# Optimization experiments

Hardware: AMD Instinct MI355X
Metric: run time of the kernel (lower is better)

Reference implementation:

```python
import jax, jax.numpy as jnp
import numpy as np

K = 9                 # kernel_size (num_points)
CENTER = K // 2
EXTEND_SCOPE = 1.0
EPS = 1e-5
GROUPS = 4            # out_ch // 4


def _cumsum_from_center(o):
    # o: [N, K, D, W, H]; serial offset accumulation outward from center row,
    # vectorized as two cumsums (matches the torch for-loop recurrence).
    upper = jnp.cumsum(o[:, CENTER:], axis=1)                                   # rows c..K-1
    lower = jnp.flip(jnp.cumsum(jnp.flip(o[:, :CENTER + 1], axis=1), axis=1), axis=1)  # rows 0..c
    return jnp.concatenate([lower[:, :CENTER], upper], axis=1)


def _coordinate_map_3d(offset):
    # offset: [N, 3K, D, W, H] -> (z, y, x) coord maps, each [N, D, W, H*K]  (morph=0, if_offset=True)
    N, _, D, W, H = offset.shape
    dt = offset.dtype
    z_off, y_off, _x_off = jnp.split(offset, 3, axis=1)   # each [N, K, D, W, H]
    z_acc = _cumsum_from_center(z_off)
    y_acc = _cumsum_from_center(y_off)
    z_c = jnp.arange(D, dtype=dt)[None, None, :, None, None]
    y_c = jnp.arange(W, dtype=dt)[None, None, None, :, None]
    x_c = jnp.arange(H, dtype=dt)[None, None, None, None, :]
    x_g = (jnp.arange(K, dtype=dt) - CENTER)[None, :, None, None, None]  # linspace(-c, c, K)
    z_new = z_c + EXTEND_SCOPE * z_acc                 # [N, K, D, W, H]
    y_new = y_c + EXTEND_SCOPE * y_acc
    x_new = jnp.broadcast_to(x_c + x_g, z_new.shape)

    def pack(a):  # [N,K,D,W,H] -> [N,D,W,H*K] (permute(0,4,1,5,2,6,3) + reshape in torch)
        return jnp.transpose(a, (0, 2, 3, 4, 1)).reshape(N, D, W, H * K)

    return pack(z_new), pack(y_new), pack(x_new)


def _trilinear_interpolate(feat, z, y, x):
    # feat: [N, C, D, W, H]; z/y/x: [N, D, W, HK] -> [N, C, D, W, HK]
    N, C, D, W, H = feat.shape
    featp = jnp.transpose(feat, (0, 2, 3, 4, 1))  # [N, D, W, H, C]
    z0 = jnp.clip(jnp.floor(z).astype(jnp.int32), 0, D - 1)
    z1 = jnp.clip(jnp.floor(z).astype(jnp.int32) + 1, 0, D - 1)
    y0 = jnp.clip(jnp.floor(y).astype(jnp.int32), 0, W - 1)
    y1 = jnp.clip(jnp.floor(y).astype(jnp.int32) + 1, 0, W - 1)
    x0 = jnp.clip(jnp.floor(x).astype(jnp.int32), 0, H - 1)
    x1 = jnp.clip(jnp.floor(x).astype(jnp.int32) + 1, 0, H - 1)
    z0f, z1f = z0.astype(feat.dtype), z1.astype(feat.dtype)
    y0f, y1f = y0.astype(feat.dtype), y1.astype(feat.dtype)
    x0f, x1f = x0.astype(feat.dtype), x1.astype(feat.dtype)
    b = jnp.arange(N)[:, None, None, None]

    def g(zi, yi, xi):
        return featp[b, zi, yi, xi]  # gather -> [N, D, W, HK, C]

    out = (g(z0, y0, x0) * ((z1f - z) * (y1f - y) * (x1f - x))[..., None]
         + g(z0, y0, x1) * ((z1f - z) * (y1f - y) * (x - x0f))[..., None]
         + g(z0, y1, x0) * ((z1f - z) * (y - y0f) * (x1f - x))[..., None]
         + g(z0, y1, x1) * ((z1f - z) * (y - y0f) * (x - x0f))[..., None]
         + g(z1, y0, x0) * ((z - z0f) * (y1f - y) * (x1f - x))[..., None]
         + g(z1, y0, x1) * ((z - z0f) * (y1f - y) * (x - x0f))[..., None]
         + g(z1, y1, x0) * ((z - z0f) * (y - y0f) * (x1f - x))[..., None]
         + g(z1, y1, x1) * ((z - z0f) * (y - y0f) * (x - x0f))[..., None])
    return jnp.transpose(out, (0, 4, 1, 2, 3))  # [N, C, D, W, HK]


def _conv3d(x, w, b, stride, padding):
    out = jax.lax.conv_general_dilated(x, w, window_strides=stride, padding=padding,
                                       dimension_numbers=('NCDHW', 'OIDHW', 'NCDHW'))
    return out + b[None, :, None, None, None]


def _batchnorm(x, gamma, beta):
    mu = jnp.mean(x, axis=(0, 2, 3, 4), keepdims=True)
    var = jnp.var(x, axis=(0, 2, 3, 4), keepdims=True)
    xn = (x - mu) * jax.lax.rsqrt(var + EPS)
    return gamma[None, :, None, None, None] * xn + beta[None, :, None, None, None]


def _groupnorm(x, gamma, beta):
    N, C = x.shape[:2]
    xg = x.reshape(N, GROUPS, C // GROUPS, *x.shape[2:])
    mu = jnp.mean(xg, axis=(2, 3, 4, 5), keepdims=True)
    var = jnp.var(xg, axis=(2, 3, 4, 5), keepdims=True)
    xn = ((xg - mu) * jax.lax.rsqrt(var + EPS)).reshape(x.shape)
    return gamma[None, :, None, None, None] * xn + beta[None, :, None, None, None]


def setup_inputs() -> dict:
    key = jax.random.key(0)
    ks = jax.random.split(key, 5)
    N, Cin, Cout, D, W, H = 1, 8, 16, 64, 64, 64
    f = jax.random.normal(ks[0], (N, Cin, D, W, H), dtype=jnp.float32)
    off_w = jax.random.normal(ks[1], (3 * K, Cin, 3, 3, 3), dtype=jnp.float32) * 0.05
    off_b = jax.random.normal(ks[2], (3 * K,), dtype=jnp.float32) * 0.05
    bn_g = jnp.ones((3 * K,), jnp.float32)
    bn_b = jnp.zeros((3 * K,), jnp.float32)
    dcn_w = jax.random.normal(ks[3], (Cout, Cin, 1, 1, K), dtype=jnp.float32) * 0.1
    dcn_b = jax.random.normal(ks[4], (Cout,), dtype=jnp.float32) * 0.05
    gn_g = jnp.ones((Cout,), jnp.float32)
    gn_b = jnp.zeros((Cout,), jnp.float32)
    return {"f": f, "off_w": off_w, "off_b": off_b, "bn_g": bn_g, "bn_b": bn_b,
            "dcn_w": dcn_w, "dcn_b": dcn_b, "gn_g": gn_g, "gn_b": gn_b}


def reference(f, off_w, off_b, bn_g, bn_b, dcn_w, dcn_b, gn_g, gn_b):
    # offset branch: Conv3d(in, 3K, 3, pad 1) -> BN -> tanh
    offset = _conv3d(f, off_w, off_b, (1, 1, 1), [(1, 1), (1, 1), (1, 1)])
    offset = jnp.tanh(_batchnorm(offset, bn_g, bn_b))
    # deformable coordinate map (morph=0) + trilinear gather
    z, y, x = _coordinate_map_3d(offset)
    deformed = _trilinear_interpolate(f, z, y, x)        # [N, C, D, W, H*K]
    # fused conv along the extended axis: kernel (1,1,K), stride (1,1,K)
    out = _conv3d(deformed, dcn_w, dcn_b, (1, 1, K), [(0, 0), (0, 0), (0, 0)])
    return jax.nn.relu(_groupnorm(out, gn_g, gn_b))      # [N, out, D, W, H]
```

## Files before the change

kernel.cpp:

```cpp
#include <hip/hip_runtime.h>
#include <math.h>

#define VOX 262144

__device__ __forceinline__ int clampi(int v, int lo, int hi) {
    return v < lo ? lo : (v > hi ? hi : v);
}

__global__ void k_init(float* __restrict__ stats) {
    if (threadIdx.x < 64) stats[threadIdx.x] = 0.f;
}

__global__ void k_wt(const float* __restrict__ w, float* __restrict__ wT) {
    int i = blockIdx.x * 256 + threadIdx.x;
    if (i < 3888) {
        int c = i / 216, r = i % 216;
        int ci = r / 27, k = r % 27;
        wT[(k * 8 + ci) * 18 + c] = w[i];
    }
}

__global__ void k_transpose(const float* __restrict__ f, float* __restrict__ ft) {
    int idx = blockIdx.x * 256 + threadIdx.x;
    int x = idx & 63, y = (idx >> 6) & 63, z = (idx >> 12) & 63, ci = idx >> 18;
    ft[(((z * 64 + y) * 64 + x) << 3) + ci] = f[idx];
}

__global__ __launch_bounds__(256) void k_conv_off(
        const float* __restrict__ f, const float* __restrict__ wT,
        const float* __restrict__ b, float* __restrict__ offs,
        float* __restrict__ stats) {
    int idx = blockIdx.x * 256 + threadIdx.x;
    int h = idx & 63, wy = (idx >> 6) & 63, d = idx >> 12;

    int hc0 = h > 0 ? h - 1 : 0;
    int hc2 = h < 63 ? h + 1 : 63;
    float mh0 = h > 0 ? 1.f : 0.f;
    float mh2 = h < 63 ? 1.f : 0.f;

    float acc[18];
#pragma unroll
    for (int c = 0; c < 18; c++) acc[c] = b[c];

#pragma unroll
    for (int kd = 0; kd < 3; kd++) {
        int dd = d + kd - 1;
#pragma unroll
        for (int kw = 0; kw < 3; kw++) {
            int ww = wy + kw - 1;
            bool ok = ((unsigned)dd < 64u) & ((unsigned)ww < 64u);
            const float* fp = f + (dd * 64 + ww) * 64;
            const float* wrow = wT + ((kd * 3 + kw) * 3) * 8 * 18;
            if (ok) {
#pragma unroll
                for (int ci = 0; ci < 8; ci++) {
                    float v0 = fp[ci * VOX + hc0] * mh0;
                    float v1 = fp[ci * VOX + h];
                    float v2 = fp[ci * VOX + hc2] * mh2;
                    const float* wp = wrow + ci * 18;
#pragma unroll
                    for (int c = 0; c < 18; c++) {
                        float a = acc[c];
                        a = fmaf(v0, wp[c], a);
                        a = fmaf(v1, wp[144 + c], a);
                        a = fmaf(v2, wp[288 + c], a);
                        acc[c] = a;
                    }
                }
            }
        }
    }

#pragma unroll
    for (int c = 0; c < 18; c++) offs[c * VOX + idx] = acc[c];

    __shared__ float ls[36];
    if (threadIdx.x < 36) ls[threadIdx.x] = 0.f;
    __syncthreads();
#pragma unroll
    for (int c = 0; c < 18; c++) {
        float s = acc[c], q = acc[c] * acc[c];
#pragma unroll
        for (int o = 32; o > 0; o >>= 1) {
            s += __shfl_xor(s, o);
            q += __shfl_xor(q, o);
        }
        if ((threadIdx.x & 63) == 0) {
            atomicAdd(&ls[c], s);
            atomicAdd(&ls[18 + c], q);
        }
    }
    __syncthreads();
    if (threadIdx.x < 36) atomicAdd(&stats[threadIdx.x], ls[threadIdx.x]);
}

__global__ __launch_bounds__(256) void k_main(
        const float* __restrict__ ft, const float* __restrict__ offs,
        const float* __restrict__ stats, const float* __restrict__ bn_g,
        const float* __restrict__ bn_b, const float* __restrict__ dw,
        const float* __restrict__ db, float* __restrict__ out,
        float* __restrict__ gstats) {
    int idx = blockIdx.x * 256 + threadIdx.x;
    int h = idx & 63, wy = (idx >> 6) & 63, d = idx >> 12;
    const float inv = 1.f / (float)VOX;

    float zo[9], yo[9];
#pragma unroll
    for (int c = 0; c < 18; c++) {
        float m = stats[c] * inv;
        float var = stats[18 + c] * inv - m * m;
        float rs = rsqrtf(var + 1e-5f);
        float t = tanhf(bn_g[c] * ((offs[c * VOX + idx] - m) * rs) + bn_b[c]);
        if (c < 9) zo[c] = t; else yo[c - 9] = t;
    }

    float za[9], ya[9];
    za[4] = zo[4]; ya[4] = yo[4];
#pragma unroll
    for (int k = 5; k < 9; k++) { za[k] = za[k - 1] + zo[k]; ya[k] = ya[k - 1] + yo[k]; }
#pragma unroll
    for (int k = 3; k >= 0; k--) { za[k] = za[k + 1] + zo[k]; ya[k] = ya[k + 1] + yo[k]; }

    float acc[16];
#pragma unroll
    for (int co = 0; co < 16; co++) acc[co] = db[co];

#pragma unroll
    for (int k = 0; k < 9; k++) {
        int xi = h + k - 4;
        if (xi >= 0 && xi <= 62) {
            float z = (float)d + za[k];
            float y = (float)wy + ya[k];
            float fz = floorf(z), fy = floorf(y);
            int iz = (int)fz, iy = (int)fy;
            int z0 = clampi(iz, 0, 63), z1 = clampi(iz + 1, 0, 63);
            int y0 = clampi(iy, 0, 63), y1 = clampi(iy + 1, 0, 63);
            float wz0 = (float)z1 - z, wz1 = z - (float)z0;
            float wy0 = (float)y1 - y, wy1 = y - (float)y0;
            float w00 = wz0 * wy0, w01 = wz0 * wy1, w10 = wz1 * wy0, w11 = wz1 * wy1;

            const float4* p00 = (const float4*)(ft + (((z0 * 64 + y0) * 64 + xi) << 3));
            const float4* p01 = (const float4*)(ft + (((z0 * 64 + y1) * 64 + xi) << 3));
            const float4* p10 = (const float4*)(ft + (((z1 * 64 + y0) * 64 + xi) << 3));
            const float4* p11 = (const float4*)(ft + (((z1 * 64 + y1) * 64 + xi) << 3));
            float4 a00 = p00[0], b00 = p00[1];
            float4 a01 = p01[0], b01 = p01[1];
            float4 a10 = p10[0], b10 = p10[1];
            float4 a11 = p11[0], b11 = p11[1];

            float v[8];
            v[0] = w00 * a00.x + w01 * a01.x + w10 * a10.x + w11 * a11.x;
            v[1] = w00 * a00.y + w01 * a01.y + w10 * a10.y + w11 * a11.y;
            v[2] = w00 * a00.z + w01 * a01.z + w10 * a10.z + w11 * a11.z;
            v[3] = w00 * a00.w + w01 * a01.w + w10 * a10.w + w11 * a11.w;
            v[4] = w00 * b00.x + w01 * b01.x + w10 * b10.x + w11 * b11.x;
            v[5] = w00 * b00.y + w01 * b01.y + w10 * b10.y + w11 * b11.y;
            v[6] = w00 * b00.z + w01 * b01.z + w10 * b10.z + w11 * b11.z;
            v[7] = w00 * b00.w + w01 * b01.w + w10 * b10.w + w11 * b11.w;

#pragma unroll
            for (int ci = 0; ci < 8; ci++) {
#pragma unroll
                for (int co = 0; co < 16; co++)
                    acc[co] = fmaf(v[ci], dw[(co * 8 + ci) * 9 + k], acc[co]);
            }
        }
    }

#pragma unroll
    for (int co = 0; co < 16; co++) out[co * VOX + idx] = acc[co];

    __shared__ float ls[8];
    if (threadIdx.x < 8) ls[threadIdx.x] = 0.f;
    __syncthreads();
#pragma unroll
    for (int g = 0; g < 4; g++) {
        float s = acc[4 * g] + acc[4 * g + 1] + acc[4 * g + 2] + acc[4 * g + 3];
        float q = acc[4 * g] * acc[4 * g] + acc[4 * g + 1] * acc[4 * g + 1]
                + acc[4 * g + 2] * acc[4 * g + 2] + acc[4 * g + 3] * acc[4 * g + 3];
#pragma unroll
        for (int o = 32; o > 0; o >>= 1) {
            s += __shfl_xor(s, o);
            q += __shfl_xor(q, o);
        }
        if ((threadIdx.x & 63) == 0) {
            atomicAdd(&ls[g], s);
            atomicAdd(&ls[4 + g], q);
        }
    }
    __syncthreads();
    if (threadIdx.x < 8) atomicAdd(&gstats[threadIdx.x], ls[threadIdx.x]);
}

__global__ void k_gn(const float* __restrict__ gstats, const float* __restrict__ gn_g,
                     const float* __restrict__ gn_b, float* __restrict__ out) {
    int idx = blockIdx.x * 256 + threadIdx.x;
    int c = idx >> 18;
    int g = c >> 2;
    const float invn = 1.f / (4.f * (float)VOX);
    float m = gstats[g] * invn;
    float var = gstats[4 + g] * invn - m * m;
    float rs = rsqrtf(var + 1e-5f);
    float v = (out[idx] - m) * rs * gn_g[c] + gn_b[c];
    out[idx] = v > 0.f ? v : 0.f;
}

extern "C" void kernel_launch(void* const* d_in, const int* in_sizes, int n_in,
                              void* d_out, int out_size, void* d_ws, size_t ws_size,
                              hipStream_t stream) {
    const float* f    = (const float*)d_in[0];
    const float* offw = (const float*)d_in[1];
    const float* offb = (const float*)d_in[2];
    const float* bng  = (const float*)d_in[3];
    const float* bnb  = (const float*)d_in[4];
    const float* dcnw = (const float*)d_in[5];
    const float* dcnb = (const float*)d_in[6];
    const float* gng  = (const float*)d_in[7];
    const float* gnb  = (const float*)d_in[8];
    float* out = (float*)d_out;

    float* ws    = (float*)d_ws;
    float* ft    = ws;
    float* offs  = ws + 8 * VOX;
    float* stats = offs + 18 * VOX;
    float* gstats = stats + 36;
    float* wT = out;

    hipLaunchKernelGGL(k_init, dim3(1), dim3(64), 0, stream, stats);
    hipLaunchKernelGGL(k_wt, dim3(16), dim3(256), 0, stream, offw, wT);
    hipLaunchKernelGGL(k_transpose, dim3((8 * VOX) / 256), dim3(256), 0, stream, f, ft);
    hipLaunchKernelGGL(k_conv_off, dim3(VOX / 256), dim3(256), 0, stream,
                       f, wT, offb, offs, stats);
    hipLaunchKernelGGL(k_main, dim3(VOX / 256), dim3(256), 0, stream,
                       ft, offs, stats, bng, bnb, dcnw, dcnb, out, gstats);
    hipLaunchKernelGGL(k_gn, dim3((16 * VOX) / 256), dim3(256), 0, stream,
                       gstats, gng, gnb, out);
}
```

Baseline: 198.3 us.

## Merge prep kernels, software-prefetch gathers, fast tanh, vectorize groupnorm

```diff
diff --git a/kernel.cpp b/kernel.cpp
--- a/kernel.cpp
+++ b/kernel.cpp
@@ -7,26 +7,29 @@
     return v < lo ? lo : (v > hi ? hi : v);
 }
 
-__global__ void k_init(float* __restrict__ stats) {
-    if (threadIdx.x < 64) stats[threadIdx.x] = 0.f;
-}
-
-__global__ void k_wt(const float* __restrict__ w, float* __restrict__ wT) {
-    int i = blockIdx.x * 256 + threadIdx.x;
-    if (i < 3888) {
-        int c = i / 216, r = i % 216;
-        int ci = r / 27, k = r % 27;
-        wT[(k * 8 + ci) * 18 + c] = w[i];
-    }
-}
-
-__global__ void k_transpose(const float* __restrict__ f, float* __restrict__ ft) {
-    int idx = blockIdx.x * 256 + threadIdx.x;
-    int x = idx & 63, y = (idx >> 6) & 63, z = (idx >> 12) & 63, ci = idx >> 18;
-    ft[(((z * 64 + y) * 64 + x) << 3) + ci] = f[idx];
-}
-
-__global__ __launch_bounds__(256) void k_conv_off(
+__global__ void k_pre(const float* __restrict__ f, float* __restrict__ ft,
+                      const float* __restrict__ w, float* __restrict__ wT,
+                      float* __restrict__ stats) {
+    int vox = blockIdx.x * 256 + threadIdx.x;
+    float v[8];
+#pragma unroll
+    for (int ci = 0; ci < 8; ci++) v[ci] = f[ci * VOX + vox];
+    float4* dst = (float4*)(ft + (size_t)vox * 8);
+    dst[0] = make_float4(v[0], v[1], v[2], v[3]);
+    dst[1] = make_float4(v[4], v[5], v[6], v[7]);
+
+    if (blockIdx.x == 0) {
+        if (threadIdx.x < 64) stats[threadIdx.x] = 0.f;
+    } else if (blockIdx.x == 1) {
+        for (int i = threadIdx.x; i < 3888; i += 256) {
+            int c = i / 216, r = i % 216;
+            int ci = r / 27, k = r % 27;
+            wT[(k * 8 + ci) * 18 + c] = w[i];
+        }
+    }
+}
+
+__global__ __launch_bounds__(256, 4) void k_conv_off(
         const float* __restrict__ f, const float* __restrict__ wT,
         const float* __restrict__ b, float* __restrict__ offs,
         float* __restrict__ stats) {
@@ -42,33 +45,49 @@
 #pragma unroll
     for (int c = 0; c < 18; c++) acc[c] = b[c];
 
-#pragma unroll
-    for (int kd = 0; kd < 3; kd++) {
-        int dd = d + kd - 1;
-#pragma unroll
-        for (int kw = 0; kw < 3; kw++) {
-            int ww = wy + kw - 1;
-            bool ok = ((unsigned)dd < 64u) & ((unsigned)ww < 64u);
-            const float* fp = f + (dd * 64 + ww) * 64;
-            const float* wrow = wT + ((kd * 3 + kw) * 3) * 8 * 18;
-            if (ok) {
-#pragma unroll
-                for (int ci = 0; ci < 8; ci++) {
-                    float v0 = fp[ci * VOX + hc0] * mh0;
-                    float v1 = fp[ci * VOX + h];
-                    float v2 = fp[ci * VOX + hc2] * mh2;
-                    const float* wp = wrow + ci * 18;
-#pragma unroll
-                    for (int c = 0; c < 18; c++) {
-                        float a = acc[c];
-                        a = fmaf(v0, wp[c], a);
-                        a = fmaf(v1, wp[144 + c], a);
-                        a = fmaf(v2, wp[288 + c], a);
-                        acc[c] = a;
-                    }
+    auto prep = [&](int s, float* V) {
+        int kd = s / 3, kw = s % 3;
+        int dc = clampi(d + kd - 1, 0, 63);
+        int wc = clampi(wy + kw - 1, 0, 63);
+        const float* fp = f + (dc * 64 + wc) * 64;
+#pragma unroll
+        for (int ci = 0; ci < 8; ci++) {
+            V[3 * ci + 0] = fp[ci * VOX + hc0];
+            V[3 * ci + 1] = fp[ci * VOX + h];
+            V[3 * ci + 2] = fp[ci * VOX + hc2];
+        }
+    };
+
+    float Va[24];
+    prep(0, Va);
+#pragma unroll
+    for (int s = 0; s < 9; s++) {
+        float Vb[24];
+        if (s < 8) prep(s + 1, Vb);
+
+        int kd = s / 3, kw = s % 3;
+        int dd = d + kd - 1, ww = wy + kw - 1;
+        bool ok = ((unsigned)dd < 64u) & ((unsigned)ww < 64u);
+        if (ok) {
+            const float* wrow = wT + s * 432;
+#pragma unroll
+            for (int ci = 0; ci < 8; ci++) {
+                float v0 = Va[3 * ci + 0] * mh0;
+                float v1 = Va[3 * ci + 1];
+                float v2 = Va[3 * ci + 2] * mh2;
+                const float* wp = wrow + ci * 18;
+#pragma unroll
+                for (int c = 0; c < 18; c++) {
+                    float a = acc[c];
+                    a = fmaf(v0, wp[c], a);
+                    a = fmaf(v1, wp[144 + c], a);
+                    a = fmaf(v2, wp[288 + c], a);
+                    acc[c] = a;
                 }
             }
         }
+#pragma unroll
+        for (int j = 0; j < 24; j++) Va[j] = Vb[j];
     }
 
 #pragma unroll
@@ -94,7 +113,7 @@
     if (threadIdx.x < 36) atomicAdd(&stats[threadIdx.x], ls[threadIdx.x]);
 }
 
-__global__ __launch_bounds__(256) void k_main(
+__global__ __launch_bounds__(256, 3) void k_main(
         const float* __restrict__ ft, const float* __restrict__ offs,
         const float* __restrict__ stats, const float* __restrict__ bn_g,
         const float* __restrict__ bn_b, const float* __restrict__ dw,
@@ -110,7 +129,10 @@
         float m = stats[c] * inv;
         float var = stats[18 + c] * inv - m * m;
         float rs = rsqrtf(var + 1e-5f);
-        float t = tanhf(bn_g[c] * ((offs[c * VOX + idx] - m) * rs) + bn_b[c]);
+        float u = bn_g[c] * ((offs[c * VOX + idx] - m) * rs) + bn_b[c];
+        u = fminf(fmaxf(u, -9.f), 9.f);
+        float e2 = __expf(2.f * u);
+        float t = (e2 - 1.f) * __builtin_amdgcn_rcpf(e2 + 1.f);
         if (c < 9) zo[c] = t; else yo[c - 9] = t;
     }
 
@@ -125,46 +147,57 @@
 #pragma unroll
     for (int co = 0; co < 16; co++) acc[co] = db[co];
 
+    auto prep = [&](int k, float4* L, float* W) {
+        int xi = h + k - 4;
+        float mk = (xi >= 0 && xi <= 62) ? 1.f : 0.f;
+        int xc = clampi(xi, 0, 62);
+        float z = (float)d + za[k];
+        float y = (float)wy + ya[k];
+        float fz = floorf(z), fy = floorf(y);
+        int iz = (int)fz, iy = (int)fy;
+        int z0 = clampi(iz, 0, 63), z1 = clampi(iz + 1, 0, 63);
+        int y0 = clampi(iy, 0, 63), y1 = clampi(iy + 1, 0, 63);
+        float wz0 = (float)z1 - z, wz1 = z - (float)z0;
+        float wyy0 = (float)y1 - y, wyy1 = y - (float)y0;
+        W[0] = wz0 * wyy0 * mk; W[1] = wz0 * wyy1 * mk;
+        W[2] = wz1 * wyy0 * mk; W[3] = wz1 * wyy1 * mk;
+        const float4* p00 = (const float4*)(ft + (((z0 * 64 + y0) * 64 + xc) << 3));
+        const float4* p01 = (const float4*)(ft + (((z0 * 64 + y1) * 64 + xc) << 3));
+        const float4* p10 = (const float4*)(ft + (((z1 * 64 + y0) * 64 + xc) << 3));
+        const float4* p11 = (const float4*)(ft + (((z1 * 64 + y1) * 64 + xc) << 3));
+        L[0] = p00[0]; L[1] = p00[1];
+        L[2] = p01[0]; L[3] = p01[1];
+        L[4] = p10[0]; L[5] = p10[1];
+        L[6] = p11[0]; L[7] = p11[1];
+    };
+
+    float4 La[8]; float Wa[4];
+    prep(0, La, Wa);
 #pragma unroll
     for (int k = 0; k < 9; k++) {
-        int xi = h + k - 4;
-        if (xi >= 0 && xi <= 62) {
-            float z = (float)d + za[k];
-            float y = (float)wy + ya[k];
-            float fz = floorf(z), fy = floorf(y);
-            int iz = (int)fz, iy = (int)fy;
-            int z0 = clampi(iz, 0, 63), z1 = clampi(iz + 1, 0, 63);
-            int y0 = clampi(iy, 0, 63), y1 = clampi(iy + 1, 0, 63);
-            float wz0 = (float)z1 - z, wz1 = z - (float)z0;
-            float wy0 = (float)y1 - y, wy1 = y - (float)y0;
-            float w00 = wz0 * wy0, w01 = wz0 * wy1, w10 = wz1 * wy0, w11 = wz1 * wy1;
-
-            const float4* p00 = (const float4*)(ft + (((z0 * 64 + y0) * 64 + xi) << 3));
-            const float4* p01 = (const float4*)(ft + (((z0 * 64 + y1) * 64 + xi) << 3));
-            const float4* p10 = (const float4*)(ft + (((z1 * 64 + y0) * 64 + xi) << 3));
-            const float4* p11 = (const float4*)(ft + (((z1 * 64 + y1) * 64 + xi) << 3));
-            float4 a00 = p00[0], b00 = p00[1];
-            float4 a01 = p01[0], b01 = p01[1];
-            float4 a10 = p10[0], b10 = p10[1];
-            float4 a11 = p11[0], b11 = p11[1];
-
-            float v[8];
-            v[0] = w00 * a00.x + w01 * a01.x + w10 * a10.x + w11 * a11.x;
-            v[1] = w00 * a00.y + w01 * a01.y + w10 * a10.y + w11 * a11.y;
-            v[2] = w00 * a00.z + w01 * a01.z + w10 * a10.z + w11 * a11.z;
-            v[3] = w00 * a00.w + w01 * a01.w + w10 * a10.w + w11 * a11.w;
-            v[4] = w00 * b00.x + w01 * b01.x + w10 * b10.x + w11 * b11.x;
-            v[5] = w00 * b00.y + w01 * b01.y + w10 * b10.y + w11 * b11.y;
-            v[6] = w00 * b00.z + w01 * b01.z + w10 * b10.z + w11 * b11.z;
-            v[7] = w00 * b00.w + w01 * b01.w + w10 * b10.w + w11 * b11.w;
-
-#pragma unroll
-            for (int ci = 0; ci < 8; ci++) {
-#pragma unroll
-                for (int co = 0; co < 16; co++)
-                    acc[co] = fmaf(v[ci], dw[(co * 8 + ci) * 9 + k], acc[co]);
-            }
-        }
+        float4 Lb[8]; float Wb[4];
+        if (k < 8) prep(k + 1, Lb, Wb);
+
+        float v[8];
+        v[0] = Wa[0] * La[0].x + Wa[1] * La[2].x + Wa[2] * La[4].x + Wa[3] * La[6].x;
+        v[1] = Wa[0] * La[0].y + Wa[1] * La[2].y + Wa[2] * La[4].y + Wa[3] * La[6].y;
+        v[2] = Wa[0] * La[0].z + Wa[1] * La[2].z + Wa[2] * La[4].z + Wa[3] * La[6].z;
+        v[3] = Wa[0] * La[0].w + Wa[1] * La[2].w + Wa[2] * La[4].w + Wa[3] * La[6].w;
+        v[4] = Wa[0] * La[1].x + Wa[1] * La[3].x + Wa[2] * La[5].x + Wa[3] * La[7].x;
+        v[5] = Wa[0] * La[1].y + Wa[1] * La[3].y + Wa[2] * La[5].y + Wa[3] * La[7].y;
+        v[6] = Wa[0] * La[1].z + Wa[1] * La[3].z + Wa[2] * La[5].z + Wa[3] * La[7].z;
+        v[7] = Wa[0] * La[1].w + Wa[1] * La[3].w + Wa[2] * La[5].w + Wa[3] * La[7].w;
+
+#pragma unroll
+        for (int ci = 0; ci < 8; ci++) {
+#pragma unroll
+            for (int co = 0; co < 16; co++)
+                acc[co] = fmaf(v[ci], dw[(co * 8 + ci) * 9 + k], acc[co]);
+        }
+#pragma unroll
+        for (int j = 0; j < 8; j++) La[j] = Lb[j];
+#pragma unroll
+        for (int j = 0; j < 4; j++) Wa[j] = Wb[j];
     }
 
 #pragma unroll
@@ -194,15 +227,20 @@
 
 __global__ void k_gn(const float* __restrict__ gstats, const float* __restrict__ gn_g,
                      const float* __restrict__ gn_b, float* __restrict__ out) {
-    int idx = blockIdx.x * 256 + threadIdx.x;
-    int c = idx >> 18;
+    int i = blockIdx.x * 256 + threadIdx.x;
+    int c = i >> 16;
     int g = c >> 2;
     const float invn = 1.f / (4.f * (float)VOX);
     float m = gstats[g] * invn;
     float var = gstats[4 + g] * invn - m * m;
     float rs = rsqrtf(var + 1e-5f);
-    float v = (out[idx] - m) * rs * gn_g[c] + gn_b[c];
-    out[idx] = v > 0.f ? v : 0.f;
+    float gg = gn_g[c], gb = gn_b[c];
+    float4 v = ((float4*)out)[i];
+    v.x = (v.x - m) * rs * gg + gb; v.x = v.x > 0.f ? v.x : 0.f;
+    v.y = (v.y - m) * rs * gg + gb; v.y = v.y > 0.f ? v.y : 0.f;
+    v.z = (v.z - m) * rs * gg + gb; v.z = v.z > 0.f ? v.z : 0.f;
+    v.w = (v.w - m) * rs * gg + gb; v.w = v.w > 0.f ? v.w : 0.f;
+    ((float4*)out)[i] = v;
 }
 
 extern "C" void kernel_launch(void* const* d_in, const int* in_sizes, int n_in,
@@ -226,13 +264,11 @@
     float* gstats = stats + 36;
     float* wT = out;
 
-    hipLaunchKernelGGL(k_init, dim3(1), dim3(64), 0, stream, stats);
-    hipLaunchKernelGGL(k_wt, dim3(16), dim3(256), 0, stream, offw, wT);
-    hipLaunchKernelGGL(k_transpose, dim3((8 * VOX) / 256), dim3(256), 0, stream, f, ft);
+    hipLaunchKernelGGL(k_pre, dim3(VOX / 256), dim3(256), 0, stream, f, ft, offw, wT, stats);
     hipLaunchKernelGGL(k_conv_off, dim3(VOX / 256), dim3(256), 0, stream,
                        f, wT, offb, offs, stats);
     hipLaunchKernelGGL(k_main, dim3(VOX / 256), dim3(256), 0, stream,
                        ft, offs, stats, bng, bnb, dcnw, dcnb, out, gstats);
-    hipLaunchKernelGGL(k_gn, dim3((16 * VOX) / 256), dim3(256), 0, stream,
+    hipLaunchKernelGGL(k_gn, dim3((16 * VOX / 4) / 256), dim3(256), 0, stream,
                        gstats, gng, gnb, out);
 }
```

New measurement: 201.1 us. No clear change (+1.4%).
